# Optimization experiments

Measured on AMD Instinct MI355X. Metric: run time of the kernel, lower is better.

## Reference

```python
import jax, jax.numpy as jnp
import numpy as np
import math

TOP_K = 2
CAP_FACTOR = 1.25
AUX_W = 0.01


def setup_inputs() -> dict:
    key = jax.random.key(0)
    k1, k2 = jax.random.split(key)
    x = jax.random.normal(k1, (8192, 4096), dtype=jnp.float32)
    # gate weight, torch init std=0.01, stored as (E, D) like nn.Linear
    gate_w = jax.random.normal(k2, (64, 4096), dtype=jnp.float32) * 0.01
    return {"x": x, "gate_w": gate_w}


def reference(x, gate_w):
    N, D = x.shape
    E = gate_w.shape[0]
    K = TOP_K
    C = max(math.ceil(CAP_FACTOR * N / E), 1)  # expert capacity

    logits = x @ gate_w.T                      # (N, E)
    probs = jax.nn.softmax(logits, axis=-1)    # (N, E)
    vals, idx = jax.lax.top_k(probs, K)        # (N, K)
    vals = vals / vals.sum(axis=-1, keepdims=True)

    # Parallel replacement of the serial double loop: flatten (N,K) row-major
    # (token-major, then k) which matches the loop iteration order exactly.
    flat_e = idx.reshape(-1)                               # (N*K,) expert ids
    oh = jax.nn.one_hot(flat_e, E, dtype=jnp.int32)        # (N*K, E)
    # exclusive prefix count of prior assignments to each expert
    pos = jnp.cumsum(oh, axis=0) - oh                      # (N*K, E)
    slot = jnp.take_along_axis(pos, flat_e[:, None], axis=1)[:, 0]  # (N*K,)
    # In the torch loop the counter saturates at C (only incremented when
    # c < C), so slot==prior_total is equivalent: kept iff prior_total < C.
    keep = slot < C
    slot_s = jnp.where(keep, slot, 0)
    tok = jnp.arange(N * K) // K

    combine_weights = jnp.zeros((N, E, C), dtype=x.dtype).at[
        tok, flat_e, slot_s].add(jnp.where(keep, vals.reshape(-1), 0.0))
    dispatch_mask = (jnp.zeros((N, E, C), dtype=jnp.int32).at[
        tok, flat_e, slot_s].add(keep.astype(jnp.int32))) > 0

    # load balancing loss
    f = oh.astype(jnp.float32).reshape(N, K, E).mean(axis=(0, 1))  # (E,)
    p = probs.mean(axis=0)                                         # (E,)
    load_loss = AUX_W * E * jnp.sum(f * p)

    return dispatch_mask, combine_weights, probs, load_loss
```

## Files before the change

### kernel.cpp

```cpp
#include <hip/hip_runtime.h>
#include <math.h>

#define N_TOK 8192
#define DIM   4096
#define NEXP  64
#define CAP   160
#define OFF_CW    (83886080ULL)
#define OFF_PROBS (167772160ULL)
#define OFF_LOSS  (168296448ULL)
#define NA    16384
#define SPLIT 8
#define KSL   (DIM / SPLIT)
#define CHUNKS (KSL / 32)

typedef short  bf16x8 __attribute__((ext_vector_type(8)));
typedef float  f32x4  __attribute__((ext_vector_type(4)));

__device__ __forceinline__ unsigned short f2bf(float f) {
    unsigned int u = __float_as_uint(f);
    return (unsigned short)((u + 0x7FFFu + ((u >> 16) & 1u)) >> 16);
}
__device__ __forceinline__ float bf2f(unsigned short h) {
    return __uint_as_float(((unsigned int)h) << 16);
}
__device__ __forceinline__ void split8(const float4 a0, const float4 a1,
                                       bf16x8& h, bf16x8& l) {
    const float v[8] = {a0.x, a0.y, a0.z, a0.w, a1.x, a1.y, a1.z, a1.w};
    #pragma unroll
    for (int e = 0; e < 8; ++e) {
        const unsigned short hh = f2bf(v[e]);
        h[e] = (short)hh;
        l[e] = (short)f2bf(v[e] - bf2f(hh));
    }
}

__device__ __forceinline__ float wave_max64(float v) {
    for (int m = 1; m < 64; m <<= 1) v = fmaxf(v, __shfl_xor(v, m, 64));
    return v;
}
__device__ __forceinline__ float wave_sum64(float v) {
    for (int m = 1; m < 64; m <<= 1) v += __shfl_xor(v, m, 64);
    return v;
}
__device__ __forceinline__ void wave_argmax64(float& v, int& i) {
    for (int m = 1; m < 64; m <<= 1) {
        float ov = __shfl_xor(v, m, 64);
        int   oi = __shfl_xor(i, m, 64);
        if (ov > v || (ov == v && oi < i)) { v = ov; i = oi; }
    }
}

__global__ __launch_bounds__(256) void k_wsplit(const float* __restrict__ gw,
                                                unsigned short* __restrict__ wh,
                                                unsigned short* __restrict__ wl) {
    const float* src = gw + (size_t)blockIdx.x * DIM;
    unsigned short* dh = wh + (size_t)blockIdx.x * DIM;
    unsigned short* dl = wl + (size_t)blockIdx.x * DIM;
    for (int i = threadIdx.x; i < DIM / 4; i += 256) {
        const float4 v = *(const float4*)(src + 4 * i);
        ushort4 h, l;
        h.x = f2bf(v.x); l.x = f2bf(v.x - bf2f(h.x));
        h.y = f2bf(v.y); l.y = f2bf(v.y - bf2f(h.y));
        h.z = f2bf(v.z); l.z = f2bf(v.z - bf2f(h.z));
        h.w = f2bf(v.w); l.w = f2bf(v.w - bf2f(h.w));
        *(ushort4*)(dh + 4 * i) = h;
        *(ushort4*)(dl + 4 * i) = l;
    }
}

__global__ __launch_bounds__(256) void k_gemm_mfma(const float* __restrict__ x,
                                                   const unsigned short* __restrict__ wh,
                                                   const unsigned short* __restrict__ wl,
                                                   float* __restrict__ part) {
    const int sy   = blockIdx.x >> 5;
    const int tb   = (blockIdx.x & 31) * 256;
    const int wv   = (threadIdx.x >> 6);
    const int lane = threadIdx.x & 63;
    const int r16  = lane & 15;
    const int kro  = (lane >> 4) * 8;
    const int tokb = tb + wv * 64;

    f32x4 acc[4][4];
    #pragma unroll
    for (int i = 0; i < 4; ++i)
        #pragma unroll
        for (int j = 0; j < 4; ++j) acc[i][j] = (f32x4){0.f, 0.f, 0.f, 0.f};

    for (int c = 0; c < CHUNKS; ++c) {
        const size_t k0 = (size_t)sy * KSL + c * 32 + kro;
        bf16x8 bhf[4], blf[4];
        #pragma unroll
        for (int j = 0; j < 4; ++j) {
            const size_t wo = (size_t)(j * 16 + r16) * DIM + k0;
            bhf[j] = *(const bf16x8*)(wh + wo);
            blf[j] = *(const bf16x8*)(wl + wo);
        }
        #pragma unroll
        for (int i = 0; i < 4; ++i) {
            const float* ap = x + (size_t)(tokb + i * 16 + r16) * DIM + k0;
            const float4 a0 = *(const float4*)(ap);
            const float4 a1 = *(const float4*)(ap + 4);
            bf16x8 ah, al;
            split8(a0, a1, ah, al);
            #pragma unroll
            for (int j = 0; j < 4; ++j) {
                acc[i][j] = __builtin_amdgcn_mfma_f32_16x16x32_bf16(ah, bhf[j], acc[i][j], 0, 0, 0);
                acc[i][j] = __builtin_amdgcn_mfma_f32_16x16x32_bf16(al, bhf[j], acc[i][j], 0, 0, 0);
                acc[i][j] = __builtin_amdgcn_mfma_f32_16x16x32_bf16(ah, blf[j], acc[i][j], 0, 0, 0);
            }
        }
    }
    float* pb = part + (size_t)sy * N_TOK * NEXP;
    #pragma unroll
    for (int i = 0; i < 4; ++i) {
        const int trow = tokb + i * 16 + (lane >> 4) * 4;
        #pragma unroll
        for (int j = 0; j < 4; ++j) {
            const int e = j * 16 + r16;
            #pragma unroll
            for (int r = 0; r < 4; ++r)
                pb[(size_t)(trow + r) * NEXP + e] = acc[i][j][r];
        }
    }
}

__global__ __launch_bounds__(256) void k_router(const float* __restrict__ part,
                                                float* __restrict__ probs_out,
                                                int* __restrict__ rec_e,
                                                float* __restrict__ rec_w) {
    const int tok  = blockIdx.x * 4 + (threadIdx.x >> 6);
    const int lane = threadIdx.x & 63;
    float l = 0.f;
    for (int s = 0; s < SPLIT; ++s)
        l += part[(size_t)s * N_TOK * NEXP + (size_t)tok * NEXP + lane];
    const float m  = wave_max64(l);
    const float ex = expf(l - m);
    const float sm = wave_sum64(ex);
    const float p  = ex / sm;
    probs_out[(size_t)tok * NEXP + lane] = p;
    float v1 = p; int i1 = lane;
    wave_argmax64(v1, i1);
    float v2 = (lane == i1) ? -1.f : p; int i2 = lane;
    wave_argmax64(v2, i2);
    if (lane == 0) {
        const float denom = v1 + v2;
        rec_e[2 * tok]     = i1;
        rec_e[2 * tok + 1] = i2;
        rec_w[2 * tok]     = v1 / denom;
        rec_w[2 * tok + 1] = v2 / denom;
    }
}

__global__ __launch_bounds__(256) void k_preduce(const float* __restrict__ probs,
                                                 float* __restrict__ psum_part) {
    __shared__ float sh[256];
    const int e = threadIdx.x & 63, tg = threadIdx.x >> 6;
    const int tok0 = blockIdx.x * 128;
    float a = 0.f;
    for (int k = 0; k < 32; ++k)
        a += probs[(size_t)(tok0 + tg + 4 * k) * NEXP + e];
    sh[threadIdx.x] = a;
    __syncthreads();
    if (threadIdx.x < 64)
        psum_part[blockIdx.x * 64 + threadIdx.x] =
            sh[threadIdx.x] + sh[64 + threadIdx.x] +
            sh[128 + threadIdx.x] + sh[192 + threadIdx.x];
}

__global__ __launch_bounds__(256) void k_assign_scatter(const int* __restrict__ rec_e,
                                                        const float* __restrict__ rec_w,
                                                        const float* __restrict__ psum_part,
                                                        float* __restrict__ out) {
    if (blockIdx.x == 16) {
        __shared__ int hcnt[64];
        if (threadIdx.x < 64) hcnt[threadIdx.x] = 0;
        __syncthreads();
        for (int j = 0; j < 64; ++j) {
            const int e = rec_e[j * 256 + threadIdx.x];
            atomicAdd(&hcnt[e], 1);
        }
        __syncthreads();
        if (threadIdx.x < 64) {
            const int e = threadIdx.x;
            float ps = 0.f;
            for (int b = 0; b < 64; ++b) ps += psum_part[b * 64 + e];
            float term = ((float)hcnt[e] / (float)NA) * (ps / (float)N_TOK);
            term = wave_sum64(term);
            if (e == 0) out[OFF_LOSS] = 0.01f * 64.f * term;
        }
        return;
    }
    const int w    = blockIdx.x * 4 + (threadIdx.x >> 6);
    const int lane = threadIdx.x & 63;
    int base = 0;
    const unsigned long long ltmask = (1ull << lane) - 1ull;
    #pragma unroll 4
    for (int c = 0; c < NA / 64; ++c) {
        const int i = c * 64 + lane;
        const int e = rec_e[i];
        const unsigned long long mask = __ballot(e == w);
        if (e == w) {
            const int slot = base + __popcll(mask & ltmask);
            if (slot < CAP) {
                const int tok = i >> 1;
                const size_t off = (size_t)tok * (NEXP * CAP) + (size_t)w * CAP + slot;
                out[off]          = 1.0f;
                out[OFF_CW + off] = rec_w[i];
            }
        }
        base += __popcll(mask);
    }
}

extern "C" void kernel_launch(void* const* d_in, const int* in_sizes, int n_in,
                              void* d_out, int out_size, void* d_ws, size_t ws_size,
                              hipStream_t stream) {
    const float* x  = (const float*)d_in[0];
    const float* gw = (const float*)d_in[1];
    float* out = (float*)d_out;

    char* w = (char*)d_ws;
    float* part      = (float*)w;
    int*   rec_e     = (int*)(w + (size_t)SPLIT * N_TOK * NEXP * 4);
    float* rec_w     = (float*)((char*)rec_e + NA * 4);
    float* psum_part = (float*)((char*)rec_w + NA * 4);
    unsigned short* wh = (unsigned short*)((char*)psum_part + 64 * 64 * 4);
    unsigned short* wl = wh + (size_t)NEXP * DIM;

    k_wsplit<<<64, 256, 0, stream>>>(gw, wh, wl);
    k_gemm_mfma<<<256, 256, 0, stream>>>(x, wh, wl, part);
    k_router<<<2048, 256, 0, stream>>>(part, out + OFF_PROBS, rec_e, rec_w);
    k_preduce<<<64, 256, 0, stream>>>(out + OFF_PROBS, psum_part);
    k_assign_scatter<<<17, 256, 0, stream>>>(rec_e, rec_w, psum_part, out);
}
```

Measured before the change: 722.4 us.

## Fuse gate GEMM, softmax, top-2 routing and prob reduction into one kernel

Replaces the weight-split, split-K GEMM, router and prob-reduce kernels with a single kernel. Each block owns 32 tokens and its four waves each cover a quarter of K. The partial logits are reduced in LDS, and softmax, top-2 selection and per-expert prob column sums are done in the same block, with the column sums combined through global atomics. This removes the large partial-logit buffer round trip through global memory and several kernel launches. In exchange every block reads and bf16-splits the full fp32 gate weight, and each wave reuses its weight fragments over only two token tiles, which adds load and conversion work per MFMA.

```diff
diff --git a/kernel.cpp b/kernel.cpp
--- a/kernel.cpp
+++ b/kernel.cpp
@@ -9,9 +9,8 @@
 #define OFF_PROBS (167772160ULL)
 #define OFF_LOSS  (168296448ULL)
 #define NA    16384
-#define SPLIT 8
-#define KSL   (DIM / SPLIT)
-#define CHUNKS (KSL / 32)
+#define TB    32
+#define KQ    1024
 
 typedef short  bf16x8 __attribute__((ext_vector_type(8)));
 typedef float  f32x4  __attribute__((ext_vector_type(4)));
@@ -50,58 +49,41 @@
     }
 }
 
-__global__ __launch_bounds__(256) void k_wsplit(const float* __restrict__ gw,
-                                                unsigned short* __restrict__ wh,
-                                                unsigned short* __restrict__ wl) {
-    const float* src = gw + (size_t)blockIdx.x * DIM;
-    unsigned short* dh = wh + (size_t)blockIdx.x * DIM;
-    unsigned short* dl = wl + (size_t)blockIdx.x * DIM;
-    for (int i = threadIdx.x; i < DIM / 4; i += 256) {
-        const float4 v = *(const float4*)(src + 4 * i);
-        ushort4 h, l;
-        h.x = f2bf(v.x); l.x = f2bf(v.x - bf2f(h.x));
-        h.y = f2bf(v.y); l.y = f2bf(v.y - bf2f(h.y));
-        h.z = f2bf(v.z); l.z = f2bf(v.z - bf2f(h.z));
-        h.w = f2bf(v.w); l.w = f2bf(v.w - bf2f(h.w));
-        *(ushort4*)(dh + 4 * i) = h;
-        *(ushort4*)(dl + 4 * i) = l;
-    }
-}
+__global__ __launch_bounds__(256) void k_fused(const float* __restrict__ x,
+                                               const float* __restrict__ gw,
+                                               float* __restrict__ probs_out,
+                                               int* __restrict__ rec_e,
+                                               float* __restrict__ rec_w,
+                                               float* __restrict__ psum_g) {
+    __shared__ float lsum[4 * TB * 65];
+    const int t    = threadIdx.x;
+    const int wv   = t >> 6;
+    const int lane = t & 63;
+    const int r16  = lane & 15;
+    const int hi4  = lane >> 4;
+    const int kro  = hi4 * 8;
+    const int tokb = blockIdx.x * TB;
+    const int kb   = wv * KQ;
 
-__global__ __launch_bounds__(256) void k_gemm_mfma(const float* __restrict__ x,
-                                                   const unsigned short* __restrict__ wh,
-                                                   const unsigned short* __restrict__ wl,
-                                                   float* __restrict__ part) {
-    const int sy   = blockIdx.x >> 5;
-    const int tb   = (blockIdx.x & 31) * 256;
-    const int wv   = (threadIdx.x >> 6);
-    const int lane = threadIdx.x & 63;
-    const int r16  = lane & 15;
-    const int kro  = (lane >> 4) * 8;
-    const int tokb = tb + wv * 64;
-
-    f32x4 acc[4][4];
+    f32x4 acc[2][4];
     #pragma unroll
-    for (int i = 0; i < 4; ++i)
+    for (int i = 0; i < 2; ++i)
         #pragma unroll
         for (int j = 0; j < 4; ++j) acc[i][j] = (f32x4){0.f, 0.f, 0.f, 0.f};
 
-    for (int c = 0; c < CHUNKS; ++c) {
-        const size_t k0 = (size_t)sy * KSL + c * 32 + kro;
+    for (int c = 0; c < KQ / 32; ++c) {
+        const size_t k0 = (size_t)kb + c * 32 + kro;
         bf16x8 bhf[4], blf[4];
         #pragma unroll
         for (int j = 0; j < 4; ++j) {
-            const size_t wo = (size_t)(j * 16 + r16) * DIM + k0;
-            bhf[j] = *(const bf16x8*)(wh + wo);
-            blf[j] = *(const bf16x8*)(wl + wo);
+            const float* gp = gw + (size_t)(j * 16 + r16) * DIM + k0;
+            split8(*(const float4*)gp, *(const float4*)(gp + 4), bhf[j], blf[j]);
         }
         #pragma unroll
-        for (int i = 0; i < 4; ++i) {
+        for (int i = 0; i < 2; ++i) {
             const float* ap = x + (size_t)(tokb + i * 16 + r16) * DIM + k0;
-            const float4 a0 = *(const float4*)(ap);
-            const float4 a1 = *(const float4*)(ap + 4);
             bf16x8 ah, al;
-            split8(a0, a1, ah, al);
+            split8(*(const float4*)ap, *(const float4*)(ap + 4), ah, al);
             #pragma unroll
             for (int j = 0; j < 4; ++j) {
                 acc[i][j] = __builtin_amdgcn_mfma_f32_16x16x32_bf16(ah, bhf[j], acc[i][j], 0, 0, 0);
@@ -110,66 +92,55 @@
             }
         }
     }
-    float* pb = part + (size_t)sy * N_TOK * NEXP;
     #pragma unroll
-    for (int i = 0; i < 4; ++i) {
-        const int trow = tokb + i * 16 + (lane >> 4) * 4;
+    for (int i = 0; i < 2; ++i)
         #pragma unroll
-        for (int j = 0; j < 4; ++j) {
-            const int e = j * 16 + r16;
+        for (int j = 0; j < 4; ++j)
             #pragma unroll
             for (int r = 0; r < 4; ++r)
-                pb[(size_t)(trow + r) * NEXP + e] = acc[i][j][r];
+                lsum[wv * (TB * 65) + (i * 16 + hi4 * 4 + r) * 65 + (j * 16 + r16)] =
+                    acc[i][j][r];
+    __syncthreads();
+    for (int f = t; f < TB * 64; f += 256) {
+        const int o = (f >> 6) * 65 + (f & 63);
+        lsum[o] = lsum[o] + lsum[TB * 65 + o] + lsum[2 * TB * 65 + o] +
+                  lsum[3 * TB * 65 + o];
+    }
+    __syncthreads();
+    float colsum = 0.f;
+    for (int q = 0; q < 8; ++q) {
+        const int tok = wv * 8 + q;
+        const float l  = lsum[tok * 65 + lane];
+        const float m  = wave_max64(l);
+        const float ex = expf(l - m);
+        const float sm = wave_sum64(ex);
+        const float p  = ex / sm;
+        probs_out[(size_t)(tokb + tok) * NEXP + lane] = p;
+        colsum += p;
+        float v1 = p; int i1 = lane;
+        wave_argmax64(v1, i1);
+        float v2 = (lane == i1) ? -1.f : p; int i2 = lane;
+        wave_argmax64(v2, i2);
+        if (lane == 0) {
+            const int gt = tokb + tok;
+            const float denom = v1 + v2;
+            rec_e[2 * gt]     = i1;
+            rec_e[2 * gt + 1] = i2;
+            rec_w[2 * gt]     = v1 / denom;
+            rec_w[2 * gt + 1] = v2 / denom;
         }
     }
-}
-
-__global__ __launch_bounds__(256) void k_router(const float* __restrict__ part,
-                                                float* __restrict__ probs_out,
-                                                int* __restrict__ rec_e,
-                                                float* __restrict__ rec_w) {
-    const int tok  = blockIdx.x * 4 + (threadIdx.x >> 6);
-    const int lane = threadIdx.x & 63;
-    float l = 0.f;
-    for (int s = 0; s < SPLIT; ++s)
-        l += part[(size_t)s * N_TOK * NEXP + (size_t)tok * NEXP + lane];
-    const float m  = wave_max64(l);
-    const float ex = expf(l - m);
-    const float sm = wave_sum64(ex);
-    const float p  = ex / sm;
-    probs_out[(size_t)tok * NEXP + lane] = p;
-    float v1 = p; int i1 = lane;
-    wave_argmax64(v1, i1);
-    float v2 = (lane == i1) ? -1.f : p; int i2 = lane;
-    wave_argmax64(v2, i2);
-    if (lane == 0) {
-        const float denom = v1 + v2;
-        rec_e[2 * tok]     = i1;
-        rec_e[2 * tok + 1] = i2;
-        rec_w[2 * tok]     = v1 / denom;
-        rec_w[2 * tok + 1] = v2 / denom;
-    }
-}
-
-__global__ __launch_bounds__(256) void k_preduce(const float* __restrict__ probs,
-                                                 float* __restrict__ psum_part) {
-    __shared__ float sh[256];
-    const int e = threadIdx.x & 63, tg = threadIdx.x >> 6;
-    const int tok0 = blockIdx.x * 128;
-    float a = 0.f;
-    for (int k = 0; k < 32; ++k)
-        a += probs[(size_t)(tok0 + tg + 4 * k) * NEXP + e];
-    sh[threadIdx.x] = a;
     __syncthreads();
-    if (threadIdx.x < 64)
-        psum_part[blockIdx.x * 64 + threadIdx.x] =
-            sh[threadIdx.x] + sh[64 + threadIdx.x] +
-            sh[128 + threadIdx.x] + sh[192 + threadIdx.x];
+    lsum[wv * 64 + lane] = colsum;
+    __syncthreads();
+    if (t < 64)
+        atomicAdd(psum_g + t,
+                  lsum[t] + lsum[64 + t] + lsum[128 + t] + lsum[192 + t]);
 }
 
 __global__ __launch_bounds__(256) void k_assign_scatter(const int* __restrict__ rec_e,
                                                         const float* __restrict__ rec_w,
-                                                        const float* __restrict__ psum_part,
+                                                        const float* __restrict__ psum_g,
                                                         float* __restrict__ out) {
     if (blockIdx.x == 16) {
         __shared__ int hcnt[64];
@@ -182,9 +153,7 @@
         __syncthreads();
         if (threadIdx.x < 64) {
             const int e = threadIdx.x;
-            float ps = 0.f;
-            for (int b = 0; b < 64; ++b) ps += psum_part[b * 64 + e];
-            float term = ((float)hcnt[e] / (float)NA) * (ps / (float)N_TOK);
+            float term = ((float)hcnt[e] / (float)NA) * (psum_g[e] / (float)N_TOK);
             term = wave_sum64(term);
             if (e == 0) out[OFF_LOSS] = 0.01f * 64.f * term;
         }
@@ -220,16 +189,11 @@
     float* out = (float*)d_out;
 
     char* w = (char*)d_ws;
-    float* part      = (float*)w;
-    int*   rec_e     = (int*)(w + (size_t)SPLIT * N_TOK * NEXP * 4);
-    float* rec_w     = (float*)((char*)rec_e + NA * 4);
-    float* psum_part = (float*)((char*)rec_w + NA * 4);
-    unsigned short* wh = (unsigned short*)((char*)psum_part + 64 * 64 * 4);
-    unsigned short* wl = wh + (size_t)NEXP * DIM;
+    int*   rec_e  = (int*)w;
+    float* rec_w  = (float*)(w + NA * 4);
+    float* psum_g = (float*)(w + 2 * NA * 4);
 
-    k_wsplit<<<64, 256, 0, stream>>>(gw, wh, wl);
-    k_gemm_mfma<<<256, 256, 0, stream>>>(x, wh, wl, part);
-    k_router<<<2048, 256, 0, stream>>>(part, out + OFF_PROBS, rec_e, rec_w);
-    k_preduce<<<64, 256, 0, stream>>>(out + OFF_PROBS, psum_part);
-    k_assign_scatter<<<17, 256, 0, stream>>>(rec_e, rec_w, psum_part, out);
+    hipMemsetAsync(psum_g, 0, NEXP * sizeof(float), stream);
+    k_fused<<<256, 256, 0, stream>>>(x, gw, out + OFF_PROBS, rec_e, rec_w, psum_g);
+    k_assign_scatter<<<17, 256, 0, stream>>>(rec_e, rec_w, psum_g, out);
 }
```

Measured after the change: 798.9 us. 10.6% more time.
